# Optimization experiments

Measured on AMD Instinct MI355X. Metric: run time of the kernel, lower is better.

The kernel has to match this reference:

```python
import jax, jax.numpy as jnp
import numpy as np

B, H, L, D, MODES = 8, 8, 4096, 64, 64
SCALE = D ** -0.5  # (d_model // n_heads) ** -0.5


def setup_inputs() -> dict:
    key = jax.random.key(0)
    kq, kk, kv = jax.random.split(key, 3)
    q = jax.random.normal(kq, (B, H, L, D), dtype=jnp.float32)
    k = jax.random.normal(kk, (B, H, L, D), dtype=jnp.float32)
    v = jax.random.normal(kv, (B, H, L, D), dtype=jnp.float32)
    # unique sorted frequency-mode indices in [0, L//2), like get_frequency_modes
    rng = np.random.default_rng(0)
    idx_q = jnp.asarray(np.sort(rng.choice(L // 2, MODES, replace=False)), dtype=jnp.int32)
    idx_k = jnp.asarray(np.sort(rng.choice(L // 2, MODES, replace=False)), dtype=jnp.int32)
    idx_v = jnp.asarray(np.sort(rng.choice(L // 2, MODES, replace=False)), dtype=jnp.int32)
    return {"q": q, "k": k, "v": v, "idx_q": idx_q, "idx_k": idx_k, "idx_v": idx_v}


def reference(q, k, v, idx_q, idx_k, idx_v):
    L_ = q.shape[2]
    # rFFT over sequence axis, then gather selected frequency modes (vectorized gather,
    # replacing the python per-index slice-assignment loop in the original)
    q_ft = jnp.fft.rfft(q, axis=2)[:, :, idx_q, :]  # [B,H,M,D] complex64
    k_ft = jnp.fft.rfft(k, axis=2)[:, :, idx_k, :]
    v_ft = jnp.fft.rfft(v, axis=2)[:, :, idx_v, :]
    # complex attention over modes; no conjugation (torch.matmul semantics)
    qk_ft = jnp.einsum('bhmd,bhnd->bhmn', q_ft, k_ft) * SCALE
    scores = jnp.tanh(qk_ft)  # complex tanh, matching torch
    values = jnp.einsum('bhmn,bhnd->bhmd', scores, v_ft)  # [B,H,M,D]
    # irfft treats the M modes as the first frequency bins, zero-padded to L//2+1
    out = jnp.fft.irfft(values, n=L_, axis=2)  # [B,H,L,D] real
    return out
```

## Files before the change

kernel.cpp:

```cpp
#include <hip/hip_runtime.h>
#include <hip/hip_bf16.h>
#include <math.h>

#define LSEQ 4096
#define DIM 64
#define TWO_PI 6.28318530717958647692f

typedef __attribute__((ext_vector_type(8))) short bf16x8;
typedef __attribute__((ext_vector_type(4))) float f32x4;


__device__ __forceinline__ unsigned short f2bfu(float f) {
  __hip_bfloat16 h = __float2bfloat16(f);
  return *(unsigned short*)&h;
}
__device__ __forceinline__ float bfu2f(unsigned short h) {
  union { unsigned int u; float f; } z;
  z.u = ((unsigned int)h) << 16;
  return z.f;
}

__global__ __launch_bounds__(256) void init_btT(unsigned short* __restrict__ btT) {
  int u = blockIdx.x * 256 + threadIdx.x;
  int l = u >> 7, kk = u & 127;
  int f = kk >> 1;
  float ang = (float)((f * l) & 4095) * (TWO_PI / 4096.0f);
  float s, c;
  sincosf(ang, &s, &c);
  float val = (kk & 1) ? -s : c;
  btT[u] = f2bfu(val);
}

__global__ __launch_bounds__(256) void init_w(unsigned short* __restrict__ whi,
                                              unsigned short* __restrict__ wlo,
                                              const int* __restrict__ iq,
                                              const int* __restrict__ ik,
                                              const int* __restrict__ iv) {
  int u = blockIdx.x * 256 + threadIdx.x;
  int tensor = u >> 19;
  int rem = u & 524287;
  int row = rem >> 12;
  int l = rem & 4095;
  int m = row & 63, reim = row >> 6;
  const int* idx = (tensor == 0 ? iq : tensor == 1 ? ik : iv);
  int f = idx[m];
  float ang = (float)((f * l) & 4095) * (TWO_PI / 4096.0f);
  float s, c;
  sincosf(ang, &s, &c);
  float val = reim ? -s : c;
  __hip_bfloat16 hb = __float2bfloat16(val);
  float fh = __bfloat162float(hb);
  whi[u] = *(unsigned short*)&hb;
  wlo[u] = f2bfu(val - fh);
}

__global__ __launch_bounds__(256) void dft_mfma(
    const float* __restrict__ q, const float* __restrict__ k,
    const float* __restrict__ v, const unsigned short* __restrict__ whi,
    const unsigned short* __restrict__ wlo, float* __restrict__ ftQK,
    unsigned short* __restrict__ ftV) {
  int b = blockIdx.x;
  int tensor = b >> 8;
  int bh = (b >> 2) & 63;
  int part = b & 3;
  const float* x =
      (tensor == 0 ? q : tensor == 1 ? k : v) + (size_t)bh * (LSEQ * DIM);
  const unsigned short* wh = whi + (size_t)tensor * 524288;
  const unsigned short* wl = wlo + (size_t)tensor * 524288;

  int t = threadIdx.x;
  int lane = t & 63, w = t >> 6;
  int l15 = lane & 15, qd = lane >> 4;
  int xd = t & 63, xseg = t >> 6;

  __shared__ __align__(16) unsigned short Wb[128 * 72];
  __shared__ __align__(16) unsigned short Xh[64 * 72];
  __shared__ __align__(16) unsigned short Xl[64 * 72];

  f32x4 acc[2][4];
#pragma unroll
  for (int mt = 0; mt < 2; ++mt)
#pragma unroll
    for (int nt = 0; nt < 4; ++nt) acc[mt][nt] = (f32x4){0.f, 0.f, 0.f, 0.f};

  bool split = (tensor != 2);
  int k0 = part * 1024;
  for (int ch = 0; ch < 16; ++ch) {
    int lc = k0 + ch * 64;
    __syncthreads();
#pragma unroll
    for (int j = 0; j < 4; ++j) {
      int u = t + 256 * j;
      int row = u >> 3, seg = u & 7;
      *(float4*)&Wb[row * 72 + seg * 8] =
          *(const float4*)&wh[(size_t)row * 4096 + lc + seg * 8];
    }
    {
      float xv[16];
#pragma unroll
      for (int i = 0; i < 16; ++i)
        xv[i] = x[(size_t)(lc + xseg * 16 + i) * 64 + xd];
      __align__(16) unsigned short hs[16];
      __align__(16) unsigned short ls[16];
#pragma unroll
      for (int i = 0; i < 16; ++i) {
        __hip_bfloat16 hb = __float2bfloat16(xv[i]);
        hs[i] = *(unsigned short*)&hb;
        float fh = __bfloat162float(hb);
        ls[i] = f2bfu(xv[i] - fh);
      }
      *(bf16x8*)&Xh[xd * 72 + xseg * 16] = *(bf16x8*)&hs[0];
      *(bf16x8*)&Xh[xd * 72 + xseg * 16 + 8] = *(bf16x8*)&hs[8];
      *(bf16x8*)&Xl[xd * 72 + xseg * 16] = *(bf16x8*)&ls[0];
      *(bf16x8*)&Xl[xd * 72 + xseg * 16 + 8] = *(bf16x8*)&ls[8];
    }
    __syncthreads();
#pragma unroll
    for (int ks = 0; ks < 2; ++ks) {
      bf16x8 af[2], bh_[4], bl_[4];
#pragma unroll
      for (int mt = 0; mt < 2; ++mt)
        af[mt] = *(const bf16x8*)&Wb[((w * 2 + mt) * 16 + l15) * 72 + ks * 32 +
                                     qd * 8];
#pragma unroll
      for (int nt = 0; nt < 4; ++nt) {
        bh_[nt] = *(const bf16x8*)&Xh[(nt * 16 + l15) * 72 + ks * 32 + qd * 8];
        bl_[nt] = *(const bf16x8*)&Xl[(nt * 16 + l15) * 72 + ks * 32 + qd * 8];
      }
#pragma unroll
      for (int mt = 0; mt < 2; ++mt)
#pragma unroll
        for (int nt = 0; nt < 4; ++nt) {
          acc[mt][nt] = __builtin_amdgcn_mfma_f32_16x16x32_bf16(
              af[mt], bh_[nt], acc[mt][nt], 0, 0, 0);
          acc[mt][nt] = __builtin_amdgcn_mfma_f32_16x16x32_bf16(
              af[mt], bl_[nt], acc[mt][nt], 0, 0, 0);
        }
    }
    if (split) {
      __syncthreads();
#pragma unroll
      for (int j = 0; j < 4; ++j) {
        int u = t + 256 * j;
        int row = u >> 3, seg = u & 7;
        *(float4*)&Wb[row * 72 + seg * 8] =
            *(const float4*)&wl[(size_t)row * 4096 + lc + seg * 8];
      }
      __syncthreads();
#pragma unroll
      for (int ks = 0; ks < 2; ++ks) {
        bf16x8 af[2], bh_[4];
#pragma unroll
        for (int mt = 0; mt < 2; ++mt)
          af[mt] = *(const bf16x8*)&Wb[((w * 2 + mt) * 16 + l15) * 72 +
                                       ks * 32 + qd * 8];
#pragma unroll
        for (int nt = 0; nt < 4; ++nt)
          bh_[nt] =
              *(const bf16x8*)&Xh[(nt * 16 + l15) * 72 + ks * 32 + qd * 8];
#pragma unroll
        for (int mt = 0; mt < 2; ++mt)
#pragma unroll
          for (int nt = 0; nt < 4; ++nt)
            acc[mt][nt] = __builtin_amdgcn_mfma_f32_16x16x32_bf16(
                af[mt], bh_[nt], acc[mt][nt], 0, 0, 0);
      }
    }
  }
  if (tensor < 2) {
    float* o = ftQK + ((size_t)(tensor * 64 + bh) * 4 + part) * 8192;
#pragma unroll
    for (int mt = 0; mt < 2; ++mt) {
      int row0 = (w * 2 + mt) * 16 + qd * 4;
#pragma unroll
      for (int nt = 0; nt < 4; ++nt) {
        int col = nt * 16 + l15;
#pragma unroll
        for (int r = 0; r < 4; ++r) o[(row0 + r) * 64 + col] = acc[mt][nt][r];
      }
    }
  } else {
    unsigned short* o = ftV + ((size_t)bh * 4 + part) * 8192;
#pragma unroll
    for (int mt = 0; mt < 2; ++mt) {
      int row0 = (w * 2 + mt) * 16 + qd * 4;
#pragma unroll
      for (int nt = 0; nt < 4; ++nt) {
        int col = nt * 16 + l15;
#pragma unroll
        for (int r = 0; r < 4; ++r)
          o[(row0 + r) * 64 + col] = f2bfu(acc[mt][nt][r]);
      }
    }
  }
}

#define FST 132
__global__ __launch_bounds__(256) void attn(const float* __restrict__ ftQK,
                                            const unsigned short* __restrict__ ftV,
                                            unsigned short* __restrict__ ypt) {
  int bh = blockIdx.x >> 2, mq = blockIdx.x & 3;
  int t = threadIdx.x;

  __shared__ float qf[16 * FST];
  __shared__ float kf[64 * FST];
  __shared__ float vf[64 * FST];
  __shared__ float S[16 * FST];

  const float* qb = ftQK + (size_t)bh * 4 * 8192;
  const float* kb = ftQK + (size_t)(64 + bh) * 4 * 8192;
  const unsigned short* vb = ftV + (size_t)bh * 4 * 8192;

#pragma unroll
  for (int j = 0; j < 8; ++j) {
    int u4 = t + 256 * j;
    int row = u4 >> 4, dq = u4 & 15;
    float4 ksum = make_float4(0.f, 0.f, 0.f, 0.f);
    float vsum[4] = {0.f, 0.f, 0.f, 0.f};
#pragma unroll
    for (int p = 0; p < 4; ++p) {
      float4 a = *(const float4*)&kb[(size_t)p * 8192 + row * 64 + dq * 4];
      ksum.x += a.x; ksum.y += a.y; ksum.z += a.z; ksum.w += a.w;
      ushort4 vv = *(const ushort4*)&vb[(size_t)p * 8192 + row * 64 + dq * 4];
      vsum[0] += bfu2f(vv.x); vsum[1] += bfu2f(vv.y);
      vsum[2] += bfu2f(vv.z); vsum[3] += bfu2f(vv.w);
    }
    int mm = row & 63, reim = row >> 6;
    int base = mm * FST + reim;
    kf[base + 2 * (4 * dq + 0)] = ksum.x;
    kf[base + 2 * (4 * dq + 1)] = ksum.y;
    kf[base + 2 * (4 * dq + 2)] = ksum.z;
    kf[base + 2 * (4 * dq + 3)] = ksum.w;
    vf[base + 2 * (4 * dq + 0)] = vsum[0];
    vf[base + 2 * (4 * dq + 1)] = vsum[1];
    vf[base + 2 * (4 * dq + 2)] = vsum[2];
    vf[base + 2 * (4 * dq + 3)] = vsum[3];
  }
#pragma unroll
  for (int j = 0; j < 2; ++j) {
    int u4 = t + 256 * j;
    int rl = u4 >> 4, dq = u4 & 15;
    int i = rl & 15, reim = rl >> 4;
    int row = reim * 64 + mq * 16 + i;
    float4 qsum = make_float4(0.f, 0.f, 0.f, 0.f);
#pragma unroll
    for (int p = 0; p < 4; ++p) {
      float4 a = *(const float4*)&qb[(size_t)p * 8192 + row * 64 + dq * 4];
      qsum.x += a.x; qsum.y += a.y; qsum.z += a.z; qsum.w += a.w;
    }
    int base = i * FST + reim;
    qf[base + 2 * (4 * dq + 0)] = qsum.x;
    qf[base + 2 * (4 * dq + 1)] = qsum.y;
    qf[base + 2 * (4 * dq + 2)] = qsum.z;
    qf[base + 2 * (4 * dq + 3)] = qsum.w;
  }
  __syncthreads();

  int m = t >> 4;
  int n0 = t & 15;
#pragma unroll
  for (int nn = 0; nn < 4; ++nn) {
    int n = n0 + 16 * nn;
    float xr = 0.0f, xi = 0.0f;
    for (int d2 = 0; d2 < 32; ++d2) {
      float4 qv = *(const float4*)&qf[m * FST + 4 * d2];
      float4 kv = *(const float4*)&kf[n * FST + 4 * d2];
      xr = fmaf(qv.x, kv.x, xr); xr = fmaf(-qv.y, kv.y, xr);
      xi = fmaf(qv.x, kv.y, xi); xi = fmaf(qv.y, kv.x, xi);
      xr = fmaf(qv.z, kv.z, xr); xr = fmaf(-qv.w, kv.w, xr);
      xi = fmaf(qv.z, kv.w, xi); xi = fmaf(qv.w, kv.z, xi);
    }
    float x = xr * 0.125f, y = xi * 0.125f;
    float tr, tim;
    if (fabsf(x) > 40.0f) {
      tr = x > 0.0f ? 1.0f : -1.0f;
      tim = 0.0f;
    } else {
      float sh = sinhf(2.0f * x), ch = coshf(2.0f * x);
      float sn, cn;
      sincosf(2.0f * y, &sn, &cn);
      float den = ch + cn;
      tr = sh / den;
      tim = sn / den;
    }
    S[m * FST + 2 * n] = tr;
    S[m * FST + 2 * n + 1] = tim;
  }
  __syncthreads();

  int d0 = t & 15;
  float ar4[4] = {0, 0, 0, 0}, ai4[4] = {0, 0, 0, 0};
  for (int n = 0; n < 64; ++n) {
    float sr_ = S[m * FST + 2 * n];
    float si_ = S[m * FST + 2 * n + 1];
    float4 va = *(const float4*)&vf[n * FST + 8 * d0];
    float4 vb2 = *(const float4*)&vf[n * FST + 8 * d0 + 4];
    ar4[0] = fmaf(sr_, va.x, ar4[0]); ar4[0] = fmaf(-si_, va.y, ar4[0]);
    ai4[0] = fmaf(sr_, va.y, ai4[0]); ai4[0] = fmaf(si_, va.x, ai4[0]);
    ar4[1] = fmaf(sr_, va.z, ar4[1]); ar4[1] = fmaf(-si_, va.w, ar4[1]);
    ai4[1] = fmaf(sr_, va.w, ai4[1]); ai4[1] = fmaf(si_, va.z, ai4[1]);
    ar4[2] = fmaf(sr_, vb2.x, ar4[2]); ar4[2] = fmaf(-si_, vb2.y, ar4[2]);
    ai4[2] = fmaf(sr_, vb2.y, ai4[2]); ai4[2] = fmaf(si_, vb2.x, ai4[2]);
    ar4[3] = fmaf(sr_, vb2.z, ar4[3]); ar4[3] = fmaf(-si_, vb2.w, ar4[3]);
    ai4[3] = fmaf(sr_, vb2.w, ai4[3]); ai4[3] = fmaf(si_, vb2.z, ai4[3]);
  }
  int fbin = mq * 16 + m;
  float cf = (fbin == 0 ? 1.0f : 2.0f) / 4096.0f;
#pragma unroll
  for (int c = 0; c < 4; ++c) {
    int d = 4 * d0 + c;
    ypt[((size_t)bh * 64 + d) * 128 + 2 * fbin] = f2bfu(cf * ar4[c]);
    ypt[((size_t)bh * 64 + d) * 128 + 2 * fbin + 1] = f2bfu(cf * ai4[c]);
  }
}

__global__ __launch_bounds__(256) void irfft_mfma(
    const unsigned short* __restrict__ ypt,
    const unsigned short* __restrict__ btT, float* __restrict__ out) {
  int bh = blockIdx.x >> 6, lc = blockIdx.x & 63;
  int t = threadIdx.x;
  int lane = t & 63, w = t >> 6;
  int l15 = lane & 15, qd = lane >> 4;

  __shared__ __align__(16) unsigned short A[2 * 64 * 72];
  __shared__ __align__(16) unsigned short Bm[2 * 64 * 72];

#pragma unroll
  for (int j = 0; j < 4; ++j) {
    int u = t + 256 * j;
    int row = u >> 4, seg = u & 15;
    int kh = seg >> 3, s8 = seg & 7;
    *(float4*)&A[kh * 4608 + row * 72 + s8 * 8] =
        *(const float4*)&btT[(size_t)(lc * 64 + row) * 128 + seg * 8];
    *(float4*)&Bm[kh * 4608 + row * 72 + s8 * 8] =
        *(const float4*)&ypt[(size_t)(bh * 64 + row) * 128 + seg * 8];
  }
  __syncthreads();

  f32x4 acc[4];
#pragma unroll
  for (int nt = 0; nt < 4; ++nt) acc[nt] = (f32x4){0.f, 0.f, 0.f, 0.f};

#pragma unroll
  for (int kh = 0; kh < 2; ++kh)
#pragma unroll
    for (int ks = 0; ks < 2; ++ks) {
      bf16x8 af =
          *(const bf16x8*)&A[kh * 4608 + (w * 16 + l15) * 72 + ks * 32 + qd * 8];
#pragma unroll
      for (int nt = 0; nt < 4; ++nt) {
        bf16x8 bf =
            *(const bf16x8*)&Bm[kh * 4608 + (nt * 16 + l15) * 72 + ks * 32 +
                                qd * 8];
        acc[nt] = __builtin_amdgcn_mfma_f32_16x16x32_bf16(af, bf, acc[nt], 0, 0, 0);
      }
    }

  float* obase = out + ((size_t)bh * 4096 + lc * 64) * 64;
  int row0 = w * 16 + qd * 4;
#pragma unroll
  for (int nt = 0; nt < 4; ++nt) {
    int col = nt * 16 + l15;
#pragma unroll
    for (int r = 0; r < 4; ++r) obase[(row0 + r) * 64 + col] = acc[nt][r];
  }
}

extern "C" void kernel_launch(void* const* d_in, const int* in_sizes, int n_in,
                              void* d_out, int out_size, void* d_ws,
                              size_t ws_size, hipStream_t stream) {
  const float* q = (const float*)d_in[0];
  const float* k = (const float*)d_in[1];
  const float* v = (const float*)d_in[2];
  const int* iq = (const int*)d_in[3];
  const int* ik = (const int*)d_in[4];
  const int* iv = (const int*)d_in[5];
  char* ws = (char*)d_ws;
  unsigned short* btT = (unsigned short*)ws;
  unsigned short* ypt = (unsigned short*)(ws + 1048576);
  float* ftQK = (float*)(ws + 2097152);
  unsigned short* ftV = (unsigned short*)(ws + 18874368);
  unsigned short* whi = (unsigned short*)(ws + 23068672);
  unsigned short* wlo = (unsigned short*)(ws + 26214400);
  float* out = (float*)d_out;

  hipLaunchKernelGGL(init_btT, dim3(2048), dim3(256), 0, stream, btT);
  hipLaunchKernelGGL(init_w, dim3(6144), dim3(256), 0, stream, whi, wlo, iq,
                     ik, iv);
  hipLaunchKernelGGL(dft_mfma, dim3(768), dim3(256), 0, stream, q, k, v, whi,
                     wlo, ftQK, ftV);
  hipLaunchKernelGGL(attn, dim3(256), dim3(256), 0, stream, ftQK, ftV, ypt);
  hipLaunchKernelGGL(irfft_mfma, dim3(4096), dim3(256), 0, stream, ypt, btT,
                     out);
}
```

Measured before the change: 266.4 us.

## Load DFT weights directly into registers and double-buffer input tiles in LDS

The forward-DFT projection kernel now loads the bf16 weight fragments (hi and lo) straight from global memory into MFMA operand registers, so the shared-memory weight staging buffer and its extra barriers are gone. The input tile is double-buffered in LDS: the next chunk's global loads are issued before the current chunk's MFMAs and converted and stored afterwards, leaving one barrier per chunk. The hi/lo weight MFMAs are merged into one loop. In exchange, register pressure rises and the direct global weight loads are less coalesced than the old staged tile loads.

```diff
diff --git a/kernel.cpp b/kernel.cpp
--- a/kernel.cpp
+++ b/kernel.cpp
@@ -73,9 +73,8 @@
   int l15 = lane & 15, qd = lane >> 4;
   int xd = t & 63, xseg = t >> 6;
 
-  __shared__ __align__(16) unsigned short Wb[128 * 72];
-  __shared__ __align__(16) unsigned short Xh[64 * 72];
-  __shared__ __align__(16) unsigned short Xl[64 * 72];
+  __shared__ __align__(16) unsigned short Xh[2][64 * 72];
+  __shared__ __align__(16) unsigned short Xl[2][64 * 72];
 
   f32x4 acc[2][4];
 #pragma unroll
@@ -85,88 +84,115 @@
 
   bool split = (tensor != 2);
   int k0 = part * 1024;
+
+  int rowA = w * 32 + l15;
+  int rowB = rowA + 16;
+  const unsigned short* wrh0 = wh + (size_t)rowA * 4096 + qd * 8;
+  const unsigned short* wrh1 = wh + (size_t)rowB * 4096 + qd * 8;
+  const unsigned short* wrl0 = wl + (size_t)rowA * 4096 + qd * 8;
+  const unsigned short* wrl1 = wl + (size_t)rowB * 4096 + qd * 8;
+
+  float xv[16];
+
+  auto cvstore = [&](int buf) {
+    __align__(16) unsigned short hs[16];
+    __align__(16) unsigned short ls[16];
+#pragma unroll
+    for (int i = 0; i < 16; ++i) {
+      __hip_bfloat16 hb = __float2bfloat16(xv[i]);
+      hs[i] = *(unsigned short*)&hb;
+      float fh = __bfloat162float(hb);
+      ls[i] = f2bfu(xv[i] - fh);
+    }
+    *(bf16x8*)&Xh[buf][xd * 72 + xseg * 16] = *(bf16x8*)&hs[0];
+    *(bf16x8*)&Xh[buf][xd * 72 + xseg * 16 + 8] = *(bf16x8*)&hs[8];
+    *(bf16x8*)&Xl[buf][xd * 72 + xseg * 16] = *(bf16x8*)&ls[0];
+    *(bf16x8*)&Xl[buf][xd * 72 + xseg * 16 + 8] = *(bf16x8*)&ls[8];
+  };
+
+  {
+    const float* xp = x + (size_t)(k0 + xseg * 16) * 64 + xd;
+#pragma unroll
+    for (int i = 0; i < 16; ++i) xv[i] = xp[(size_t)i * 64];
+  }
+  cvstore(0);
+
+#pragma unroll 2
   for (int ch = 0; ch < 16; ++ch) {
     int lc = k0 + ch * 64;
+    int cur = ch & 1;
+
+    bf16x8 afh[2][2], afl[2][2];
+#pragma unroll
+    for (int ks = 0; ks < 2; ++ks) {
+      afh[0][ks] = *(const bf16x8*)(wrh0 + lc + ks * 32);
+      afh[1][ks] = *(const bf16x8*)(wrh1 + lc + ks * 32);
+    }
+    if (split) {
+#pragma unroll
+      for (int ks = 0; ks < 2; ++ks) {
+        afl[0][ks] = *(const bf16x8*)(wrl0 + lc + ks * 32);
+        afl[1][ks] = *(const bf16x8*)(wrl1 + lc + ks * 32);
+      }
+    }
+
+    if (ch < 15) {
+      const float* xp = x + (size_t)(lc + 64 + xseg * 16) * 64 + xd;
+#pragma unroll
+      for (int i = 0; i < 16; ++i) xv[i] = xp[(size_t)i * 64];
+    }
+
     __syncthreads();
-#pragma unroll
-    for (int j = 0; j < 4; ++j) {
-      int u = t + 256 * j;
-      int row = u >> 3, seg = u & 7;
-      *(float4*)&Wb[row * 72 + seg * 8] =
-          *(const float4*)&wh[(size_t)row * 4096 + lc + seg * 8];
-    }
-    {
-      float xv[16];
-#pragma unroll
-      for (int i = 0; i < 16; ++i)
-        xv[i] = x[(size_t)(lc + xseg * 16 + i) * 64 + xd];
-      __align__(16) unsigned short hs[16];
-      __align__(16) unsigned short ls[16];
-#pragma unroll
-      for (int i = 0; i < 16; ++i) {
-        __hip_bfloat16 hb = __float2bfloat16(xv[i]);
-        hs[i] = *(unsigned short*)&hb;
-        float fh = __bfloat162float(hb);
-        ls[i] = f2bfu(xv[i] - fh);
-      }
-      *(bf16x8*)&Xh[xd * 72 + xseg * 16] = *(bf16x8*)&hs[0];
-      *(bf16x8*)&Xh[xd * 72 + xseg * 16 + 8] = *(bf16x8*)&hs[8];
-      *(bf16x8*)&Xl[xd * 72 + xseg * 16] = *(bf16x8*)&ls[0];
-      *(bf16x8*)&Xl[xd * 72 + xseg * 16 + 8] = *(bf16x8*)&ls[8];
-    }
-    __syncthreads();
-#pragma unroll
-    for (int ks = 0; ks < 2; ++ks) {
-      bf16x8 af[2], bh_[4], bl_[4];
-#pragma unroll
-      for (int mt = 0; mt < 2; ++mt)
-        af[mt] = *(const bf16x8*)&Wb[((w * 2 + mt) * 16 + l15) * 72 + ks * 32 +
-                                     qd * 8];
-#pragma unroll
-      for (int nt = 0; nt < 4; ++nt) {
-        bh_[nt] = *(const bf16x8*)&Xh[(nt * 16 + l15) * 72 + ks * 32 + qd * 8];
-        bl_[nt] = *(const bf16x8*)&Xl[(nt * 16 + l15) * 72 + ks * 32 + qd * 8];
-      }
-#pragma unroll
-      for (int mt = 0; mt < 2; ++mt)
+
+    if (split) {
+#pragma unroll
+      for (int ks = 0; ks < 2; ++ks) {
+        bf16x8 bh_[4], bl_[4];
 #pragma unroll
         for (int nt = 0; nt < 4; ++nt) {
-          acc[mt][nt] = __builtin_amdgcn_mfma_f32_16x16x32_bf16(
-              af[mt], bh_[nt], acc[mt][nt], 0, 0, 0);
-          acc[mt][nt] = __builtin_amdgcn_mfma_f32_16x16x32_bf16(
-              af[mt], bl_[nt], acc[mt][nt], 0, 0, 0);
+          bh_[nt] =
+              *(const bf16x8*)&Xh[cur][(nt * 16 + l15) * 72 + ks * 32 + qd * 8];
+          bl_[nt] =
+              *(const bf16x8*)&Xl[cur][(nt * 16 + l15) * 72 + ks * 32 + qd * 8];
         }
-    }
-    if (split) {
-      __syncthreads();
-#pragma unroll
-      for (int j = 0; j < 4; ++j) {
-        int u = t + 256 * j;
-        int row = u >> 3, seg = u & 7;
-        *(float4*)&Wb[row * 72 + seg * 8] =
-            *(const float4*)&wl[(size_t)row * 4096 + lc + seg * 8];
-      }
-      __syncthreads();
+#pragma unroll
+        for (int mt = 0; mt < 2; ++mt)
+#pragma unroll
+          for (int nt = 0; nt < 4; ++nt) {
+            acc[mt][nt] = __builtin_amdgcn_mfma_f32_16x16x32_bf16(
+                afh[mt][ks], bh_[nt], acc[mt][nt], 0, 0, 0);
+            acc[mt][nt] = __builtin_amdgcn_mfma_f32_16x16x32_bf16(
+                afh[mt][ks], bl_[nt], acc[mt][nt], 0, 0, 0);
+            acc[mt][nt] = __builtin_amdgcn_mfma_f32_16x16x32_bf16(
+                afl[mt][ks], bh_[nt], acc[mt][nt], 0, 0, 0);
+          }
+      }
+    } else {
 #pragma unroll
       for (int ks = 0; ks < 2; ++ks) {
-        bf16x8 af[2], bh_[4];
+        bf16x8 bh_[4], bl_[4];
+#pragma unroll
+        for (int nt = 0; nt < 4; ++nt) {
+          bh_[nt] =
+              *(const bf16x8*)&Xh[cur][(nt * 16 + l15) * 72 + ks * 32 + qd * 8];
+          bl_[nt] =
+              *(const bf16x8*)&Xl[cur][(nt * 16 + l15) * 72 + ks * 32 + qd * 8];
+        }
 #pragma unroll
         for (int mt = 0; mt < 2; ++mt)
-          af[mt] = *(const bf16x8*)&Wb[((w * 2 + mt) * 16 + l15) * 72 +
-                                       ks * 32 + qd * 8];
-#pragma unroll
-        for (int nt = 0; nt < 4; ++nt)
-          bh_[nt] =
-              *(const bf16x8*)&Xh[(nt * 16 + l15) * 72 + ks * 32 + qd * 8];
-#pragma unroll
-        for (int mt = 0; mt < 2; ++mt)
-#pragma unroll
-          for (int nt = 0; nt < 4; ++nt)
+#pragma unroll
+          for (int nt = 0; nt < 4; ++nt) {
             acc[mt][nt] = __builtin_amdgcn_mfma_f32_16x16x32_bf16(
-                af[mt], bh_[nt], acc[mt][nt], 0, 0, 0);
-      }
-    }
-  }
+                afh[mt][ks], bh_[nt], acc[mt][nt], 0, 0, 0);
+            acc[mt][nt] = __builtin_amdgcn_mfma_f32_16x16x32_bf16(
+                afh[mt][ks], bl_[nt], acc[mt][nt], 0, 0, 0);
+          }
+      }
+    }
+
+    if (ch < 15) cvstore(cur ^ 1);
+  }
+
   if (tensor < 2) {
     float* o = ftQK + ((size_t)(tensor * 64 + bh) * 4 + part) * 8192;
 #pragma unroll
```

Result: no change. 262.5 us (-1.4%).
